# Optimization experiments

Hardware: AMD Instinct MI355X
Metric: run time of the kernel (lower is better)

The kernel has to match this reference:

```python
import jax, jax.numpy as jnp
import numpy as np

D_MODEL = 1024
N_HEADS = 16
HEAD_DIM = D_MODEL // N_HEADS
WINDOW = 256


def setup_inputs() -> dict:
    key = jax.random.key(0)
    k1, k2, k3 = jax.random.split(key, 3)
    x = jax.random.normal(k1, (1, 4096, D_MODEL), dtype=jnp.float32)
    # torch nn.Linear weights: [out_features, in_features]
    W_qkv = jax.random.normal(k2, (3 * D_MODEL, D_MODEL), dtype=jnp.float32) * (D_MODEL ** -0.5)
    W_proj = jax.random.normal(k3, (D_MODEL, D_MODEL), dtype=jnp.float32) * (D_MODEL ** -0.5)
    return {"x": x, "W_qkv": W_qkv, "W_proj": W_proj}


def reference(x, W_qkv, W_proj):
    B, T, D = x.shape
    H, Hd = N_HEADS, HEAD_DIM
    qkv = (x @ W_qkv.T).reshape(B, T, 3, H, Hd)
    qkv = jnp.transpose(qkv, (2, 0, 3, 1, 4))  # [3, B, H, T, Hd]
    q, k, v = qkv[0], qkv[1], qkv[2]
    # causal + sliding-window mask: allowed iff 0 <= i - j < WINDOW
    i = jnp.arange(T)[:, None]
    j = jnp.arange(T)[None, :]
    mask = (j <= i) & (j >= i - (WINDOW - 1))  # [T, T] bool
    scale = Hd ** -0.5
    attn = jnp.einsum('bhid,bhjd->bhij', q, k) * scale
    attn = jnp.where(mask, attn, -jnp.inf)
    attn = jax.nn.softmax(attn, axis=-1)
    out = jnp.einsum('bhij,bhjd->bhid', attn, v)  # [B, H, T, Hd]
    out = jnp.transpose(out, (0, 2, 1, 3)).reshape(B, T, D)
    return out @ W_proj.T
```

## Files before the change

### kernel.cpp

```cpp
#include <hip/hip_runtime.h>
#include <hip/hip_bf16.h>


#define T_SEQ   4096
#define DM      1024
#define NH      16
#define HD      64
#define WIN     256

typedef unsigned short u16_t;
typedef u16_t  u16v8 __attribute__((ext_vector_type(8)));
typedef __bf16 bf16v8 __attribute__((ext_vector_type(8)));
typedef float  f32v4 __attribute__((ext_vector_type(4)));

__device__ __forceinline__ f32v4 mfma_bf16(u16v8 a, u16v8 b, f32v4 c) {
    return __builtin_amdgcn_mfma_f32_16x16x32_bf16(
        __builtin_bit_cast(bf16v8, a), __builtin_bit_cast(bf16v8, b), c, 0, 0, 0);
}

__device__ __forceinline__ u16_t f2bf(float f) {
    unsigned u = __builtin_bit_cast(unsigned, f);
    u += 0x7fffu + ((u >> 16) & 1u);
    return (u16_t)(u >> 16);
}

__device__ __forceinline__ float exp2_fast(float x) {
    return __builtin_amdgcn_exp2f(x);
}

__device__ __forceinline__ void gload_lds16(const u16_t* g, u16_t* l) {
    __builtin_amdgcn_global_load_lds(
        (const __attribute__((address_space(1))) unsigned int*)g,
        (__attribute__((address_space(3))) unsigned int*)l, 16, 0, 0);
}

__global__ void cvt_kernel(const float* __restrict__ in, u16_t* __restrict__ out, int n8) {
    int i = blockIdx.x * blockDim.x + threadIdx.x;
    if (i >= n8) return;
    const float4* p = (const float4*)(in + (size_t)i * 8);
    float4 a = p[0], b = p[1];
    u16v8 o;
    o[0] = f2bf(a.x); o[1] = f2bf(a.y); o[2] = f2bf(a.z); o[3] = f2bf(a.w);
    o[4] = f2bf(b.x); o[5] = f2bf(b.y); o[6] = f2bf(b.z); o[7] = f2bf(b.w);
    *(u16v8*)(out + (size_t)i * 8) = o;
}

template <int BM, int BN, int WN, int WAVES, typename OutT>
__global__ __launch_bounds__(WAVES * 64, 2)
void gemm_ring(const u16_t* __restrict__ A, const u16_t* __restrict__ B,
               OutT* __restrict__ C, int M, int N, int K) {
    constexpr int WM  = WAVES / WN;
    constexpr int PWM = BM / WM;
    constexpr int PWN = BN / WN;
    constexpr int M_F = PWM / 16, N_F = PWN / 16;
    constexpr int N_H = N_F / 2;
    constexpr int THREADS = WAVES * 64;
    constexpr int RP = THREADS / 4;

    __shared__ u16_t lA[4 * BM * 32];
    __shared__ u16_t lB[4 * BN * 32];

    const int tid = threadIdx.x;
    const int l = tid & 63, w = tid >> 6;
    const int lr = l & 15, g = l >> 4;
    const int wrh = w / WN, wcq = w % WN;
    const int arow0 = blockIdx.y * BM, bcol0 = blockIdx.x * BN;
    const int rq = tid >> 2, cq = tid & 3;
    const int NS = K >> 5;

    f32v4 acc[M_F][N_F];
#pragma unroll
    for (int m = 0; m < M_F; ++m)
#pragma unroll
        for (int n = 0; n < N_F; ++n) acc[m][n] = f32v4{0.f, 0.f, 0.f, 0.f};

#define GSTAGE(s_)                                                                      \
    do {                                                                                \
        const int k0_ = (s_) << 5, sl_ = (s_) & 3;                                      \
        _Pragma("unroll")                                                               \
        for (int p = 0; p < BM / RP; ++p) {                                             \
            int r = rq + p * RP;                                                        \
            int cs = cq ^ ((r >> 1) & 3);                                               \
            gload_lds16(A + (size_t)(arow0 + r) * K + k0_ + cs * 8,                     \
                        lA + sl_ * (BM * 32) + r * 32 + cq * 8);                        \
        }                                                                               \
        _Pragma("unroll")                                                               \
        for (int p = 0; p < BN / RP; ++p) {                                             \
            int r = rq + p * RP;                                                        \
            int cs = cq ^ ((r >> 1) & 3);                                               \
            gload_lds16(B + (size_t)(bcol0 + r) * K + k0_ + cs * 8,                     \
                        lB + sl_ * (BN * 32) + r * 32 + cq * 8);                        \
        }                                                                               \
    } while (0)

    GSTAGE(0); GSTAGE(1); GSTAGE(2);

    for (int s = 0; s < NS; ++s) {
        if (s < NS - 2)       { asm volatile("s_waitcnt vmcnt(8)" ::: "memory"); }
        else if (s == NS - 2) { asm volatile("s_waitcnt vmcnt(4)" ::: "memory"); }
        else                  { asm volatile("s_waitcnt vmcnt(0)" ::: "memory"); }
        __builtin_amdgcn_s_barrier();
        __builtin_amdgcn_sched_barrier(0);
        if (s + 3 < NS) GSTAGE(s + 3);

        const u16_t* sA = lA + (s & 3) * (BM * 32);
        const u16_t* sB = lB + (s & 3) * (BN * 32);
        u16v8 a[M_F], b[N_F];
#pragma unroll
        for (int mf = 0; mf < M_F; ++mf) {
            int row = wrh * PWM + mf * 16 + lr;
            a[mf] = *(const u16v8*)(sA + row * 32 + (g ^ ((row >> 1) & 3)) * 8);
        }
#pragma unroll
        for (int nf = 0; nf < N_H; ++nf) {
            int row = wcq * PWN + nf * 16 + lr;
            b[nf] = *(const u16v8*)(sB + row * 32 + (g ^ ((row >> 1) & 3)) * 8);
        }
        __builtin_amdgcn_s_setprio(1);
#pragma unroll
        for (int mf = 0; mf < M_F; ++mf)
#pragma unroll
            for (int nf = 0; nf < N_H; ++nf)
                acc[mf][nf] = mfma_bf16(a[mf], b[nf], acc[mf][nf]);
        __builtin_amdgcn_s_setprio(0);
#pragma unroll
        for (int nf = N_H; nf < N_F; ++nf) {
            int row = wcq * PWN + nf * 16 + lr;
            b[nf] = *(const u16v8*)(sB + row * 32 + (g ^ ((row >> 1) & 3)) * 8);
        }
        __builtin_amdgcn_s_setprio(1);
#pragma unroll
        for (int mf = 0; mf < M_F; ++mf)
#pragma unroll
            for (int nf = N_H; nf < N_F; ++nf)
                acc[mf][nf] = mfma_bf16(a[mf], b[nf], acc[mf][nf]);
        __builtin_amdgcn_s_setprio(0);
    }
#undef GSTAGE

#pragma unroll
    for (int mf = 0; mf < M_F; ++mf) {
        int crow0 = arow0 + wrh * PWM + mf * 16 + g * 4;
#pragma unroll
        for (int nf = 0; nf < N_F; ++nf) {
            int ccol = bcol0 + wcq * PWN + nf * 16 + lr;
#pragma unroll
            for (int j = 0; j < 4; ++j) {
                float v = acc[mf][nf][j];
                if constexpr (sizeof(OutT) == 2)
                    C[(size_t)(crow0 + j) * N + ccol] = (OutT)f2bf(v);
                else
                    C[(size_t)(crow0 + j) * N + ccol] = (OutT)v;
            }
        }
    }
}

__global__ __launch_bounds__(256) void vtrans_kernel(const u16_t* __restrict__ qkv,
                                                     u16_t* __restrict__ vt) {
    __shared__ u16_t tile[64][72];
    const int t0 = blockIdx.x * 64, h = blockIdx.y;
    const int tid = threadIdx.x;
    {
        int r = tid >> 2, c = (tid & 3) * 16;
        const u16_t* src = qkv + (size_t)(t0 + r) * (3 * DM) + 2 * DM + h * HD + c;
        *(u16v8*)&tile[r][c]     = *(const u16v8*)src;
        *(u16v8*)&tile[r][c + 8] = *(const u16v8*)(src + 8);
    }
    __syncthreads();
    {
        int d = tid >> 2, ts = (tid & 3) * 16;
        u16_t* dst = vt + ((size_t)h * HD + d) * T_SEQ + t0 + ts;
        u16v8 o0, o1;
#pragma unroll
        for (int i = 0; i < 8; ++i) { o0[i] = tile[ts + i][d]; o1[i] = tile[ts + 8 + i][d]; }
        *(u16v8*)dst       = o0;
        *(u16v8*)(dst + 8) = o1;
    }
}

__global__ __launch_bounds__(256) void attn_kernel(const u16_t* __restrict__ qkv,
                                                   const u16_t* __restrict__ vt,
                                                   u16_t* __restrict__ out) {
    __shared__ u16_t lK[2][64 * 64];
    __shared__ u16_t lV[2][64 * 64];
    __shared__ u16_t pbuf[4][16 * 64];

    const int h = blockIdx.y;
    const int q0 = blockIdx.x * 64;
    const int tid = threadIdx.x;
    const int w = tid >> 6, l = tid & 63;
    const int lr = l & 15, g = l >> 4;
    const int i0 = q0 + w * 16;
    u16_t* P = pbuf[w];

    const int r_st = tid >> 3;
    const int c8l  = tid & 7;
    const u16_t* kBase = qkv + DM + h * HD;
    const u16_t* vBase = vt + (size_t)h * HD * T_SEQ;

    u16v8 qf0, qf1;
    {
        const u16_t* qrow = qkv + h * HD + (size_t)(i0 + lr) * (3 * DM) + g * 8;
        qf0 = *(const u16v8*)qrow;
        qf1 = *(const u16v8*)(qrow + 32);
    }
    f32v4 o[4];
#pragma unroll
    for (int n = 0; n < 4; ++n) o[n] = f32v4{0.f, 0.f, 0.f, 0.f};
    float m_run[4], l_run[4];
#pragma unroll
    for (int j = 0; j < 4; ++j) { m_run[j] = -1e30f; l_run[j] = 0.f; }

    const int c0 = (q0 >= WIN) ? q0 - WIN : 0;
    const int nch = ((q0 - c0) >> 6) + 1;

#define STAGE_KV(buf, cc)                                                              \
    do {                                                                               \
        _Pragma("unroll")                                                              \
        for (int p = 0; p < 2; ++p) {                                                  \
            int rr = r_st + p * 32;                                                    \
            int cs = c8l ^ (rr & 7);                                                   \
            gload_lds16(kBase + (size_t)(cc + rr) * (3 * DM) + cs * 8,                 \
                        lK[buf] + (size_t)(rr * 64 + c8l * 8));                        \
            gload_lds16(vBase + (size_t)rr * T_SEQ + (cc) + cs * 8,                    \
                        lV[buf] + (size_t)(rr * 64 + c8l * 8));                        \
        }                                                                              \
    } while (0)

    STAGE_KV(0, c0);

    const float sc = 0.125f * 1.4426950408889634f;

    for (int ci = 0; ci < nch; ++ci) {
        const int c = c0 + (ci << 6);
        const int cur = ci & 1;
        __syncthreads();
        if (ci + 1 < nch) STAGE_KV(cur ^ 1, c + 64);

        const u16_t* K = lK[cur];
        const u16_t* V = lV[cur];

        f32v4 s[4];
#pragma unroll
        for (int kt = 0; kt < 4; ++kt) {
            int krow = kt * 16 + lr;
            u16v8 k0 = *(const u16v8*)(K + krow * 64 + ((g     ^ (krow & 7)) * 8));
            u16v8 k1 = *(const u16v8*)(K + krow * 64 + (((4+g) ^ (krow & 7)) * 8));
            f32v4 z = f32v4{0.f, 0.f, 0.f, 0.f};
            z = mfma_bf16(qf0, k0, z);
            z = mfma_bf16(qf1, k1, z);
            s[kt] = z;
        }

        const bool full = (c + 63 <= i0) && (c >= i0 - 240);
        if (full) {
#pragma unroll
            for (int kt = 0; kt < 4; ++kt)
#pragma unroll
                for (int j = 0; j < 4; ++j) s[kt][j] *= sc;
        } else {
#pragma unroll
            for (int j = 0; j < 4; ++j) {
                const int i = i0 + g * 4 + j;
#pragma unroll
                for (int kt = 0; kt < 4; ++kt) {
                    const int jg = c + kt * 16 + lr;
                    float v = s[kt][j] * sc;
                    const bool okm = (jg <= i) && (jg >= i - (WIN - 1));
                    s[kt][j] = okm ? v : -3e38f;
                }
            }
        }

        float mloc[4], corr[4], rsum[4];
#pragma unroll
        for (int j = 0; j < 4; ++j)
            mloc[j] = fmaxf(fmaxf(s[0][j], s[1][j]), fmaxf(s[2][j], s[3][j]));
#pragma unroll
        for (int d = 1; d < 16; d <<= 1)
#pragma unroll
            for (int j = 0; j < 4; ++j) mloc[j] = fmaxf(mloc[j], __shfl_xor(mloc[j], d, 64));
#pragma unroll
        for (int j = 0; j < 4; ++j) {
            float mnew = fmaxf(m_run[j], mloc[j]);
            corr[j] = exp2_fast(m_run[j] - mnew);
            m_run[j] = mnew;
            rsum[j] = 0.f;
        }
#pragma unroll
        for (int kt = 0; kt < 4; ++kt)
#pragma unroll
            for (int j = 0; j < 4; ++j) {
                float p = exp2_fast(s[kt][j] - m_run[j]);
                rsum[j] += p;
                int rP = g * 4 + j;
                int col = kt * 16 + lr;
                int c8 = col >> 3;
                P[rP * 64 + ((c8 ^ (rP & 7)) * 8 + (col & 7))] = f2bf(p);
            }
#pragma unroll
        for (int d = 1; d < 16; d <<= 1)
#pragma unroll
            for (int j = 0; j < 4; ++j) rsum[j] += __shfl_xor(rsum[j], d, 64);
#pragma unroll
        for (int j = 0; j < 4; ++j) l_run[j] = l_run[j] * corr[j] + rsum[j];
#pragma unroll
        for (int n = 0; n < 4; ++n)
#pragma unroll
            for (int j = 0; j < 4; ++j) o[n][j] *= corr[j];

        u16v8 pa0 = *(const u16v8*)(P + lr * 64 + ((g     ^ (lr & 7)) * 8));
        u16v8 pa1 = *(const u16v8*)(P + lr * 64 + (((4+g) ^ (lr & 7)) * 8));
#pragma unroll
        for (int n = 0; n < 4; ++n) {
            int vrow = n * 16 + lr;
            u16v8 v0 = *(const u16v8*)(V + vrow * 64 + ((g     ^ (vrow & 7)) * 8));
            u16v8 v1 = *(const u16v8*)(V + vrow * 64 + (((4+g) ^ (vrow & 7)) * 8));
            o[n] = mfma_bf16(pa0, v0, o[n]);
            o[n] = mfma_bf16(pa1, v1, o[n]);
        }
    }
#undef STAGE_KV

#pragma unroll
    for (int n = 0; n < 4; ++n)
#pragma unroll
        for (int j = 0; j < 4; ++j) {
            int t = i0 + g * 4 + j;
            out[(size_t)t * DM + h * HD + n * 16 + lr] = f2bf(o[n][j] / l_run[j]);
        }
}

extern "C" void kernel_launch(void* const* d_in, const int* in_sizes, int n_in,
                              void* d_out, int out_size, void* d_ws, size_t ws_size,
                              hipStream_t stream) {
    const float* x     = (const float*)d_in[0];
    const float* wqkv  = (const float*)d_in[1];
    const float* wproj = (const float*)d_in[2];
    float* out = (float*)d_out;
    char* ws = (char*)d_ws;

    u16_t* xb     = (u16_t*)(ws);
    u16_t* wqkvb  = (u16_t*)(ws + (size_t)(8u << 20));
    u16_t* wprojb = (u16_t*)(ws + (size_t)(14u << 20));
    u16_t* qkvb   = (u16_t*)(ws + (size_t)(16u << 20));
    u16_t* vt     = (u16_t*)(ws + (size_t)(40u << 20));
    u16_t* attnb  = (u16_t*)(ws);

    const int n8x = T_SEQ * DM / 8, n8q = 3 * DM * DM / 8, n8p = DM * DM / 8;
    cvt_kernel<<<(n8x + 255) / 256, 256, 0, stream>>>(x, xb, n8x);
    cvt_kernel<<<(n8q + 255) / 256, 256, 0, stream>>>(wqkv, wqkvb, n8q);
    cvt_kernel<<<(n8p + 255) / 256, 256, 0, stream>>>(wproj, wprojb, n8p);

    gemm_ring<256, 256, 4, 8, u16_t><<<dim3(3 * DM / 256, T_SEQ / 256), 512, 0, stream>>>(
        xb, wqkvb, qkvb, T_SEQ, 3 * DM, DM);

    vtrans_kernel<<<dim3(T_SEQ / 64, NH), 256, 0, stream>>>(qkvb, vt);

    attn_kernel<<<dim3(T_SEQ / 64, NH), 256, 0, stream>>>(qkvb, vt, attnb);

    gemm_ring<128, 128, 2, 4, float><<<dim3(DM / 128, T_SEQ / 128), 256, 0, stream>>>(
        attnb, wprojb, out, T_SEQ, DM, DM);
}
```

Before: 182.0 us.

## Replace 4-stage LDS ring GEMM with double-buffered GEMM and smaller tiles

```diff
diff --git a/kernel.cpp b/kernel.cpp
--- a/kernel.cpp
+++ b/kernel.cpp
@@ -45,20 +45,19 @@
     *(u16v8*)(out + (size_t)i * 8) = o;
 }
 
-template <int BM, int BN, int WN, int WAVES, typename OutT>
-__global__ __launch_bounds__(WAVES * 64, 2)
-void gemm_ring(const u16_t* __restrict__ A, const u16_t* __restrict__ B,
-               OutT* __restrict__ C, int M, int N, int K) {
+template <int BM, int BN, int WN, int WAVES, int MW, typename OutT>
+__global__ __launch_bounds__(WAVES * 64, MW)
+void gemm2p(const u16_t* __restrict__ A, const u16_t* __restrict__ B,
+            OutT* __restrict__ C, int M, int N, int K) {
     constexpr int WM  = WAVES / WN;
     constexpr int PWM = BM / WM;
     constexpr int PWN = BN / WN;
     constexpr int M_F = PWM / 16, N_F = PWN / 16;
-    constexpr int N_H = N_F / 2;
     constexpr int THREADS = WAVES * 64;
-    constexpr int RP = THREADS / 4;
-
-    __shared__ u16_t lA[4 * BM * 32];
-    __shared__ u16_t lB[4 * BN * 32];
+    constexpr int RPP = THREADS / 4;
+
+    __shared__ u16_t lA[2][BM * 32];
+    __shared__ u16_t lB[2][BN * 32];
 
     const int tid = threadIdx.x;
     const int l = tid & 63, w = tid >> 6;
@@ -66,7 +65,7 @@
     const int wrh = w / WN, wcq = w % WN;
     const int arow0 = blockIdx.y * BM, bcol0 = blockIdx.x * BN;
     const int rq = tid >> 2, cq = tid & 3;
-    const int NS = K >> 5;
+    const int NT = K >> 5;
 
     f32v4 acc[M_F][N_F];
 #pragma unroll
@@ -74,37 +73,33 @@
 #pragma unroll
         for (int n = 0; n < N_F; ++n) acc[m][n] = f32v4{0.f, 0.f, 0.f, 0.f};
 
-#define GSTAGE(s_)                                                                      \
+#define GSTAGE(buf, kt0)                                                                \
     do {                                                                                \
-        const int k0_ = (s_) << 5, sl_ = (s_) & 3;                                      \
         _Pragma("unroll")                                                               \
-        for (int p = 0; p < BM / RP; ++p) {                                             \
-            int r = rq + p * RP;                                                        \
+        for (int p = 0; p < BM / RPP; ++p) {                                            \
+            int r = rq + p * RPP;                                                       \
             int cs = cq ^ ((r >> 1) & 3);                                               \
-            gload_lds16(A + (size_t)(arow0 + r) * K + k0_ + cs * 8,                     \
-                        lA + sl_ * (BM * 32) + r * 32 + cq * 8);                        \
+            gload_lds16(A + (size_t)(arow0 + r) * K + (kt0) + cs * 8,                   \
+                        lA[buf] + r * 32 + cq * 8);                                     \
         }                                                                               \
         _Pragma("unroll")                                                               \
-        for (int p = 0; p < BN / RP; ++p) {                                             \
-            int r = rq + p * RP;                                                        \
+        for (int p = 0; p < BN / RPP; ++p) {                                            \
+            int r = rq + p * RPP;                                                       \
             int cs = cq ^ ((r >> 1) & 3);                                               \
-            gload_lds16(B + (size_t)(bcol0 + r) * K + k0_ + cs * 8,                     \
-                        lB + sl_ * (BN * 32) + r * 32 + cq * 8);                        \
+            gload_lds16(B + (size_t)(bcol0 + r) * K + (kt0) + cs * 8,                   \
+                        lB[buf] + r * 32 + cq * 8);                                     \
         }                                                                               \
     } while (0)
 
-    GSTAGE(0); GSTAGE(1); GSTAGE(2);
-
-    for (int s = 0; s < NS; ++s) {
-        if (s < NS - 2)       { asm volatile("s_waitcnt vmcnt(8)" ::: "memory"); }
-        else if (s == NS - 2) { asm volatile("s_waitcnt vmcnt(4)" ::: "memory"); }
-        else                  { asm volatile("s_waitcnt vmcnt(0)" ::: "memory"); }
-        __builtin_amdgcn_s_barrier();
+    GSTAGE(0, 0);
+    __syncthreads();
+
+    for (int t = 0; t < NT; ++t) {
+        if (t + 1 < NT) GSTAGE((t + 1) & 1, (t + 1) << 5);
         __builtin_amdgcn_sched_barrier(0);
-        if (s + 3 < NS) GSTAGE(s + 3);
-
-        const u16_t* sA = lA + (s & 3) * (BM * 32);
-        const u16_t* sB = lB + (s & 3) * (BN * 32);
+
+        const u16_t* sA = lA[t & 1];
+        const u16_t* sB = lB[t & 1];
         u16v8 a[M_F], b[N_F];
 #pragma unroll
         for (int mf = 0; mf < M_F; ++mf) {
@@ -112,7 +107,7 @@
             a[mf] = *(const u16v8*)(sA + row * 32 + (g ^ ((row >> 1) & 3)) * 8);
         }
 #pragma unroll
-        for (int nf = 0; nf < N_H; ++nf) {
+        for (int nf = 0; nf < N_F; ++nf) {
             int row = wcq * PWN + nf * 16 + lr;
             b[nf] = *(const u16v8*)(sB + row * 32 + (g ^ ((row >> 1) & 3)) * 8);
         }
@@ -120,21 +115,11 @@
 #pragma unroll
         for (int mf = 0; mf < M_F; ++mf)
 #pragma unroll
-            for (int nf = 0; nf < N_H; ++nf)
+            for (int nf = 0; nf < N_F; ++nf)
                 acc[mf][nf] = mfma_bf16(a[mf], b[nf], acc[mf][nf]);
         __builtin_amdgcn_s_setprio(0);
-#pragma unroll
-        for (int nf = N_H; nf < N_F; ++nf) {
-            int row = wcq * PWN + nf * 16 + lr;
-            b[nf] = *(const u16v8*)(sB + row * 32 + (g ^ ((row >> 1) & 3)) * 8);
-        }
-        __builtin_amdgcn_s_setprio(1);
-#pragma unroll
-        for (int mf = 0; mf < M_F; ++mf)
-#pragma unroll
-            for (int nf = N_H; nf < N_F; ++nf)
-                acc[mf][nf] = mfma_bf16(a[mf], b[nf], acc[mf][nf]);
-        __builtin_amdgcn_s_setprio(0);
+
+        __syncthreads();
     }
 #undef GSTAGE
 
@@ -353,13 +338,13 @@
     cvt_kernel<<<(n8q + 255) / 256, 256, 0, stream>>>(wqkv, wqkvb, n8q);
     cvt_kernel<<<(n8p + 255) / 256, 256, 0, stream>>>(wproj, wprojb, n8p);
 
-    gemm_ring<256, 256, 4, 8, u16_t><<<dim3(3 * DM / 256, T_SEQ / 256), 512, 0, stream>>>(
+    gemm2p<128, 128, 2, 4, 3, u16_t><<<dim3(3 * DM / 128, T_SEQ / 128), 256, 0, stream>>>(
         xb, wqkvb, qkvb, T_SEQ, 3 * DM, DM);
 
     vtrans_kernel<<<dim3(T_SEQ / 64, NH), 256, 0, stream>>>(qkvb, vt);
 
     attn_kernel<<<dim3(T_SEQ / 64, NH), 256, 0, stream>>>(qkvb, vt, attnb);
 
-    gemm_ring<128, 128, 2, 4, float><<<dim3(DM / 128, T_SEQ / 128), 256, 0, stream>>>(
+    gemm2p<64, 128, 2, 4, 2, float><<<dim3(DM / 128, T_SEQ / 64), 256, 0, stream>>>(
         attnb, wprojb, out, T_SEQ, DM, DM);
 }
```

New measurement: 165.1 us. -9.3%, faster.
